# Kernel optimization log

Hardware: AMD Instinct MI355X
Metric: run time of the kernel (lower is better)

The kernel has to match this reference:

```python
import jax, jax.numpy as jnp
import numpy as np

N_ENT = 100000
N_REL = 100
DIM = 128
N_BASES = 10
N_LAYERS = 2
N_EDGES = 600000


def setup_inputs() -> dict:
    key = jax.random.key(0)
    ks = jax.random.split(key, 8)
    source = jax.random.randint(ks[0], (N_EDGES,), 0, N_ENT)
    target = jax.random.randint(ks[1], (N_EDGES,), 0, N_ENT)
    edge_type = jax.random.randint(ks[2], (N_EDGES,), 0, N_REL)
    x0 = jax.random.normal(ks[3], (N_ENT, DIM), dtype=jnp.float32)
    bases = jax.random.normal(ks[4], (N_BASES, DIM, DIM), dtype=jnp.float32) * (DIM ** -0.5)
    coefs = jax.random.normal(ks[5], (N_LAYERS, N_REL, N_BASES), dtype=jnp.float32) * (N_BASES ** -0.5)
    self_w = jax.random.normal(ks[6], (N_LAYERS, DIM, DIM), dtype=jnp.float32) * (DIM ** -0.5)
    bias = jnp.zeros((N_LAYERS, DIM), dtype=jnp.float32)
    return {"x0": x0, "bases": bases, "coefs": coefs, "self_w": self_w,
            "bias": bias, "source": source, "target": target, "edge_type": edge_type}


def reference(x0, bases, coefs, self_w, bias, source, target, edge_type):
    """R-GCN entity representations (basis decomposition, inverse in-degree norm).

    x0: (N, d) base entity embeddings; bases: (B, d, d); coefs: (L, R, B);
    self_w: (L, d, d); bias: (L, d); source/target/edge_type: (E,) int.
    Returns (N, d) entity representations after L layers.
    """
    n = x0.shape[0]
    n_layers = coefs.shape[0]
    n_bases = bases.shape[0]
    # inverse in-degree edge weights: w_e = 1 / indegree(target_e)
    indeg = jax.ops.segment_sum(jnp.ones_like(target, dtype=x0.dtype), target, num_segments=n)
    ew = (1.0 / jnp.maximum(indeg, 1.0))[target]  # (E,)
    x = x0
    for l in range(n_layers):
        xs = x[source]                         # (E, d) gather
        ecoef = coefs[l][edge_type]            # (E, B) relation-specific basis coefficients
        msg = jnp.zeros_like(xs)
        for b in range(n_bases):               # small fixed loop over bases
            msg = msg + ecoef[:, b:b + 1] * (xs @ bases[b])
        agg = jax.ops.segment_sum(ew[:, None] * msg, target, num_segments=n)  # (N, d)
        x = jax.nn.relu(agg + x @ self_w[l] + bias[l])
    return x
```

## Files before the change

### kernel.cpp

```cpp
#include <hip/hip_runtime.h>

#define NENT    100000
#define NENTPAD 100096
#define NREL    100
#define DIM     128
#define NBASES  10
#define NEDGES  600000
#define CH      128
#define TMAX    4788
#define PADE    612736
#define NB_ESCAN 98
#define EPB     4096
#define NBH     147
#define NPERS   512

typedef unsigned short u16;
typedef unsigned int   u32;
typedef __bf16  bf16x8 __attribute__((ext_vector_type(8)));
typedef float   f32x16 __attribute__((ext_vector_type(16)));

static __device__ __forceinline__ u16 f2bf(float f) {
  u32 u = __float_as_uint(f);
  u = (u + 0x7fffu + ((u >> 16) & 1u)) >> 16;
  return (u16)u;
}
static __device__ __forceinline__ float bf2f(u32 h) {
  return __uint_as_float(h << 16);
}
static __device__ __forceinline__ u32 pk2(float a, float b) {
  return (u32)f2bf(a) | ((u32)f2bf(b) << 16);
}
#define GLD16(g, l) __builtin_amdgcn_global_load_lds( \
    (__attribute__((address_space(1))) u32*)(g), \
    (__attribute__((address_space(3))) u32*)(l), 16, 0, 0)

__global__ __launch_bounds__(1024) void k_hist2(const int* __restrict__ tgt,
                                                const int* __restrict__ rel,
                                                int* __restrict__ indeg,
                                                int* __restrict__ hist) {
  __shared__ int h[NREL];
  int tid = threadIdx.x, blk = blockIdx.x;
  if (tid < NREL) h[tid] = 0;
  __syncthreads();
  int base = blk * EPB;
  int nv = NEDGES - base; if (nv > EPB) nv = EPB;
#pragma unroll
  for (int k = 0; k < 4; ++k) {
    int j = tid + k * 1024;
    if (j < nv) {
      int i = base + j;
      atomicAdd(&indeg[tgt[i]], 1);
      atomicAdd(&h[rel[i]], 1);
    }
  }
  __syncthreads();
  if (tid < NREL) hist[tid * NBH + blk] = h[tid];
}

__global__ __launch_bounds__(1024) void k_scan2(int* __restrict__ hist,
                                                int* __restrict__ chunk_rel,
                                                int* __restrict__ chunk_start,
                                                int* __restrict__ chunk_valid,
                                                int* __restrict__ chunkT) {
  __shared__ int sh[NREL * NBH];
  __shared__ int cnt[NREL];
  __shared__ int cb[128];
  int tid = threadIdx.x;
  for (int i = tid; i < NREL * NBH; i += 1024) sh[i] = hist[i];
  __syncthreads();
  if (tid < NREL) {
    int s = 0;
    for (int b = 0; b < NBH; ++b) s += sh[tid * NBH + b];
    cnt[tid] = s;
  }
  __syncthreads();
  if (tid < 128) cb[tid] = (tid < NREL) ? (cnt[tid] + CH - 1) / CH : 0;
  __syncthreads();
  for (int d = 1; d < 128; d <<= 1) {
    int t = 0;
    if (tid < 128 && tid >= d) t = cb[tid - d];
    __syncthreads();
    if (tid < 128) cb[tid] += t;
    __syncthreads();
  }
  if (tid < NREL) {
    int c = cnt[tid];
    int nch = (c + CH - 1) / CH;
    int cb0 = cb[tid] - nch;
    int poff = cb0 * CH;
    for (int i = 0; i < nch; ++i) {
      chunk_rel[cb0 + i] = tid;
      chunk_start[cb0 + i] = (cb0 + i) * CH;
      int v = c - i * CH;
      if (v > CH) v = CH;
      chunk_valid[cb0 + i] = v;
    }
    int run = poff;
    for (int b = 0; b < NBH; ++b) {
      int t = sh[tid * NBH + b];
      sh[tid * NBH + b] = run;
      run += t;
    }
  }
  if (tid == 127) *chunkT = cb[127];
  __syncthreads();
  for (int i = tid; i < NREL * NBH; i += 1024) hist[i] = sh[i];
}

__global__ __launch_bounds__(1024) void k_scatter2(const int* __restrict__ src,
                                                   const int* __restrict__ tgt,
                                                   const int* __restrict__ rel,
                                                   const int* __restrict__ hist,
                                                   const int* __restrict__ row_ptr,
                                                   int* __restrict__ fill_t,
                                                   int* __restrict__ es,
                                                   int* __restrict__ tp) {
  __shared__ int lh[NREL];
  __shared__ int lc[NREL];
  __shared__ int goff[NREL];
  __shared__ int ls[128];
  __shared__ int es_l[EPB];
  __shared__ int tp_l[EPB];
  __shared__ int dst_l[EPB];
  int tid = threadIdx.x, blk = blockIdx.x;
  int base = blk * EPB;
  int nv = NEDGES - base; if (nv > EPB) nv = EPB;
  if (tid < NREL) {
    lh[tid] = 0; lc[tid] = 0;
    goff[tid] = hist[tid * NBH + blk];
  }
  __syncthreads();
  int r4[4], s4[4], t4[4];
#pragma unroll
  for (int k = 0; k < 4; ++k) {
    int j = tid + k * 1024;
    if (j < nv) {
      int i = base + j;
      r4[k] = rel[i]; s4[k] = src[i]; t4[k] = tgt[i];
      atomicAdd(&lh[r4[k]], 1);
    } else r4[k] = -1;
  }
  __syncthreads();
  if (tid < 128) ls[tid] = (tid < NREL) ? lh[tid] : 0;
  __syncthreads();
  for (int d = 1; d < 128; d <<= 1) {
    int t = 0;
    if (tid < 128 && tid >= d) t = ls[tid - d];
    __syncthreads();
    if (tid < 128) ls[tid] += t;
    __syncthreads();
  }
#pragma unroll
  for (int k = 0; k < 4; ++k) {
    if (r4[k] >= 0) {
      int r = r4[k];
      int rank = atomicAdd(&lc[r], 1);
      int lpos = ls[r] - lh[r] + rank;
      es_l[lpos] = s4[k];
      dst_l[lpos] = goff[r] + rank;
      tp_l[lpos] = row_ptr[t4[k]] + atomicAdd(&fill_t[t4[k]], 1);
    }
  }
  __syncthreads();
  for (int j = tid; j < nv; j += 1024) {
    int d = dst_l[j];
    es[d] = es_l[j];
    tp[d] = tp_l[j];
  }
}

__global__ void k_escanA(const int* __restrict__ indeg, int* __restrict__ loc,
                         int* __restrict__ bsum) {
  __shared__ int s[256];
  int tid = threadIdx.x;
  int base = blockIdx.x * 1024 + tid * 4;
  int v0 = (base + 0 < NENT) ? indeg[base + 0] : 0;
  int v1 = (base + 1 < NENT) ? indeg[base + 1] : 0;
  int v2 = (base + 2 < NENT) ? indeg[base + 2] : 0;
  int v3 = (base + 3 < NENT) ? indeg[base + 3] : 0;
  s[tid] = v0 + v1 + v2 + v3;
  __syncthreads();
  for (int d = 1; d < 256; d <<= 1) {
    int t = (tid >= d) ? s[tid - d] : 0;
    __syncthreads();
    s[tid] += t;
    __syncthreads();
  }
  int off = (tid > 0) ? s[tid - 1] : 0;
  if (base + 0 < NENT) loc[base + 0] = off;
  if (base + 1 < NENT) loc[base + 1] = off + v0;
  if (base + 2 < NENT) loc[base + 2] = off + v0 + v1;
  if (base + 3 < NENT) loc[base + 3] = off + v0 + v1 + v2;
  if (tid == 255) bsum[blockIdx.x] = s[255];
}

__global__ void k_escanB(int* __restrict__ bsum) {
  __shared__ int s[128];
  int tid = threadIdx.x;
  s[tid] = (tid < NB_ESCAN) ? bsum[tid] : 0;
  __syncthreads();
  for (int d = 1; d < 128; d <<= 1) {
    int t = (tid >= d) ? s[tid - d] : 0;
    __syncthreads();
    s[tid] += t;
    __syncthreads();
  }
  if (tid < NB_ESCAN) bsum[tid] = (tid > 0) ? s[tid - 1] : 0;
}

__global__ void k_escanC(const int* __restrict__ loc, const int* __restrict__ bsum,
                         int* __restrict__ row_ptr) {
  int i = blockIdx.x * blockDim.x + threadIdx.x;
  if (i < NENT) row_ptr[i] = loc[i] + bsum[i >> 10];
}

__global__ void k_tobf(const float* __restrict__ x, u16* __restrict__ xbf) {
  int t = blockIdx.x * 256 + threadIdx.x;
  int row = t >> 4, g = t & 15;
  int c = g ^ (row & 7);
  const float4* xr = (const float4*)(x + (size_t)row * DIM + c * 8);
  float4 a = xr[0], b = xr[1];
  uint4 o;
  o.x = pk2(a.x, a.y); o.y = pk2(a.z, a.w);
  o.z = pk2(b.x, b.y); o.w = pk2(b.z, b.w);
  *(uint4*)(xbf + (size_t)row * DIM + g * 8) = o;
}

__global__ void k_wmatT(const float* __restrict__ bases, const float* __restrict__ coefs_l,
                        u16* __restrict__ Wt) {
  int g = blockIdx.x * 256 + threadIdx.x;
  int r = g >> 11;
  int rem = g & 2047;
  int k8 = rem >> 7;
  int dim = rem & 127;
  float cf[NBASES];
#pragma unroll
  for (int bb = 0; bb < NBASES; ++bb) cf[bb] = coefs_l[r * NBASES + bb];
  float v[8];
#pragma unroll
  for (int i = 0; i < 8; ++i) v[i] = 0.f;
  for (int bb = 0; bb < NBASES; ++bb) {
    const float* bp = bases + (size_t)bb * DIM * DIM + (k8 * 8) * DIM + dim;
#pragma unroll
    for (int i = 0; i < 8; ++i) v[i] += cf[bb] * bp[i * DIM];
  }
  uint4 o;
  o.x = pk2(v[0], v[1]); o.y = pk2(v[2], v[3]);
  o.z = pk2(v[4], v[5]); o.w = pk2(v[6], v[7]);
  *(uint4*)(Wt + (size_t)r * DIM * DIM + dim * DIM + ((k8 ^ (dim & 7)) * 8)) = o;
}

__global__ void k_swtT(const float* __restrict__ sw, u16* __restrict__ swt) {
  int g = blockIdx.x * 256 + threadIdx.x;
  int ll = g >> 11;
  int rem = g & 2047;
  int k8 = rem >> 7;
  int dim = rem & 127;
  const float* bp = sw + (size_t)ll * DIM * DIM + (k8 * 8) * DIM + dim;
  float v[8];
#pragma unroll
  for (int i = 0; i < 8; ++i) v[i] = bp[i * DIM];
  uint4 o;
  o.x = pk2(v[0], v[1]); o.y = pk2(v[2], v[3]);
  o.z = pk2(v[4], v[5]); o.w = pk2(v[6], v[7]);
  *(uint4*)(swt + (size_t)ll * DIM * DIM + dim * DIM + ((k8 ^ (dim & 7)) * 8)) = o;
}

__launch_bounds__(512, 2)
__global__ void k_edgeP(const u16* __restrict__ xbf, const u16* __restrict__ Wt,
                        const int* __restrict__ es, const int* __restrict__ tp,
                        const int* __restrict__ chunk_rel, const int* __restrict__ chunk_start,
                        const int* __restrict__ chunk_valid, const int* __restrict__ chunkT,
                        u16* __restrict__ msg) {
  __shared__ __align__(16) char smem[65536];
  int nch = *chunkT;
  int K = (nch + NPERS - 1) / NPERS;
  int c0 = blockIdx.x * K;
  int c1 = c0 + K; if (c1 > nch) c1 = nch;
  if (c0 >= nch) return;
  int tid = threadIdx.x;
  int w = tid >> 6, l = tid & 63;
  int lr = l & 31, hi = l >> 5;
  int dt = w & 3;
  int d = dt * 32 + lr;
  int e1 = (w >> 2) * 32 + lr;
  int aswz = d & 7, bswz = lr & 7;
  const char* wb = smem;
  const char* xb = smem + 32768;
  int curR = -1;
  for (int cb = c0; cb < c1; ++cb) {
    int r = chunk_rel[cb], base = chunk_start[cb], nv = chunk_valid[cb];
    __syncthreads();
    if (r != curR) {
      const char* wg = (const char*)(Wt + (size_t)r * DIM * DIM);
#pragma unroll
      for (int it = 0; it < 4; ++it) {
        int off = it * 8192 + tid * 16;
        GLD16(wg + off, smem + off);
      }
      curR = r;
    }
    {
      int e = tid >> 2, q = tid & 3;
      int sidx = (e < nv) ? es[base + e] : 0;
      const char* xr = (const char*)(xbf + (size_t)sidx * DIM);
      char* xd = smem + 32768 + e * 256;
      int xk = (sidx & 7) ^ (e & 7);
#pragma unroll
      for (int i = 0; i < 4; ++i) {
        int g = q * 4 + i;
        uint4 v = *(const uint4*)(xr + g * 16);
        *(uint4*)(xd + ((g ^ xk) * 16)) = v;
      }
    }
    __syncthreads();
    f32x16 accA, accB;
#pragma unroll
    for (int i = 0; i < 16; ++i) { accA[i] = 0.f; accB[i] = 0.f; }
#pragma unroll
    for (int s = 0; s < 8; ++s) {
      int c = s * 2 + hi;
      bf16x8 av = *(const bf16x8*)(wb + d * 256 + ((c ^ aswz) * 16));
      bf16x8 b1 = *(const bf16x8*)(xb + e1 * 256 + ((c ^ bswz) * 16));
      bf16x8 b2 = *(const bf16x8*)(xb + (e1 + 64) * 256 + ((c ^ bswz) * 16));
      accA = __builtin_amdgcn_mfma_f32_32x32x16_bf16(av, b1, accA, 0, 0, 0);
      accB = __builtin_amdgcn_mfma_f32_32x32x16_bf16(av, b2, accB, 0, 0, 0);
    }
#pragma unroll
    for (int t = 0; t < 2; ++t) {
      int e = e1 + t * 64;
      if (e < nv) {
        int p = tp[base + e];
        u16* mrow = msg + (size_t)p * DIM + dt * 32 + hi * 16;
#pragma unroll
        for (int half = 0; half < 2; ++half) {
          float v0 = t ? accB[8 * half + 0] : accA[8 * half + 0];
          float v1 = t ? accB[8 * half + 1] : accA[8 * half + 1];
          float v2 = t ? accB[8 * half + 2] : accA[8 * half + 2];
          float v3 = t ? accB[8 * half + 3] : accA[8 * half + 3];
          float v4 = t ? accB[8 * half + 4] : accA[8 * half + 4];
          float v5 = t ? accB[8 * half + 5] : accA[8 * half + 5];
          float v6 = t ? accB[8 * half + 6] : accA[8 * half + 6];
          float v7 = t ? accB[8 * half + 7] : accA[8 * half + 7];
          uint4 o;
          o.x = pk2(v0, v1); o.y = pk2(v2, v3);
          o.z = pk2(v4, v5); o.w = pk2(v6, v7);
          *(uint4*)(mrow + 8 * half) = o;
        }
      }
    }
  }
}

#define ACC8(M, B_) \
  ms[(B_) + 0] += bf2f((M).x & 0xffffu); ms[(B_) + 1] += bf2f((M).x >> 16); \
  ms[(B_) + 2] += bf2f((M).y & 0xffffu); ms[(B_) + 3] += bf2f((M).y >> 16); \
  ms[(B_) + 4] += bf2f((M).z & 0xffffu); ms[(B_) + 5] += bf2f((M).z >> 16); \
  ms[(B_) + 6] += bf2f((M).w & 0xffffu); ms[(B_) + 7] += bf2f((M).w >> 16);

__launch_bounds__(512, 4)
__global__ void k_combM(const u16* __restrict__ xbf, const u16* __restrict__ swt,
                        const float* __restrict__ bias_l, const u16* __restrict__ msg,
                        const int* __restrict__ row_ptr, const int* __restrict__ indeg,
                        float* __restrict__ outf, u16* __restrict__ outb, int last) {
  __shared__ __align__(16) char smem[65536];
  int tid = threadIdx.x;
  int r0 = blockIdx.x * 128;
  {
    const char* wg = (const char*)swt;
    const char* xg = (const char*)(xbf + (size_t)r0 * DIM);
#pragma unroll
    for (int it = 0; it < 4; ++it) {
      int off = it * 8192 + tid * 16;
      GLD16(wg + off, smem + off);
      GLD16(xg + off, smem + 32768 + off);
    }
  }
  __syncthreads();
  int w = tid >> 6, l = tid & 63;
  int lr = l & 31, hi = l >> 5;
  int dt = w & 3;
  int d = dt * 32 + lr;
  int e1 = (w >> 2) * 32 + lr;
  const char* wb = smem;
  const char* xb = smem + 32768;
  f32x16 accA, accB;
#pragma unroll
  for (int i = 0; i < 16; ++i) { accA[i] = 0.f; accB[i] = 0.f; }
  int aswz = d & 7, bswz = lr & 7;
#pragma unroll
  for (int s = 0; s < 8; ++s) {
    int c = s * 2 + hi;
    bf16x8 av = *(const bf16x8*)(wb + d * 256 + ((c ^ aswz) * 16));
    bf16x8 b1 = *(const bf16x8*)(xb + e1 * 256 + ((c ^ bswz) * 16));
    bf16x8 b2 = *(const bf16x8*)(xb + (e1 + 64) * 256 + ((c ^ bswz) * 16));
    accA = __builtin_amdgcn_mfma_f32_32x32x16_bf16(av, b1, accA, 0, 0, 0);
    accB = __builtin_amdgcn_mfma_f32_32x32x16_bf16(av, b2, accB, 0, 0, 0);
  }
#pragma unroll
  for (int t = 0; t < 2; ++t) {
    int ent = r0 + e1 + t * 64;
    int vald = (ent < NENT);
    int eb = vald ? row_ptr[ent] : 0;
    int dg = vald ? indeg[ent] : 0;
    float inv = 1.f / (float)(dg > 1 ? dg : 1);
    float ms[16];
#pragma unroll
    for (int i = 0; i < 16; ++i) ms[i] = 0.f;
    const u16* mp = msg + (size_t)eb * DIM + dt * 32 + hi * 16;
    int j = 0;
    for (; j + 1 < dg; j += 2) {
      uint4 m1 = *(const uint4*)(mp);
      uint4 m2 = *(const uint4*)(mp + 8);
      uint4 m3 = *(const uint4*)(mp + DIM);
      uint4 m4 = *(const uint4*)(mp + DIM + 8);
      ACC8(m1, 0) ACC8(m2, 8) ACC8(m3, 0) ACC8(m4, 8)
      mp += 2 * DIM;
    }
    if (j < dg) {
      uint4 m1 = *(const uint4*)(mp);
      uint4 m2 = *(const uint4*)(mp + 8);
      ACC8(m1, 0) ACC8(m2, 8)
    }
    if (vald) {
#pragma unroll
      for (int q = 0; q < 4; ++q) {
        float4 bi = *(const float4*)(bias_l + dt * 32 + hi * 4 + 8 * q);
        float a0 = t ? accB[4 * q + 0] : accA[4 * q + 0];
        float a1 = t ? accB[4 * q + 1] : accA[4 * q + 1];
        float a2 = t ? accB[4 * q + 2] : accA[4 * q + 2];
        float a3 = t ? accB[4 * q + 3] : accA[4 * q + 3];
        float o0 = fmaxf(ms[4 * q + 0] * inv + a0 + bi.x, 0.f);
        float o1 = fmaxf(ms[4 * q + 1] * inv + a1 + bi.y, 0.f);
        float o2 = fmaxf(ms[4 * q + 2] * inv + a2 + bi.z, 0.f);
        float o3 = fmaxf(ms[4 * q + 3] * inv + a3 + bi.w, 0.f);
        if (last) {
          float4 o = make_float4(o0, o1, o2, o3);
          *(float4*)(outf + (size_t)ent * DIM + dt * 32 + hi * 4 + 8 * q) = o;
        } else {
          int c16 = 4 * dt + q;
          uint2 o;
          o.x = pk2(o0, o1); o.y = pk2(o2, o3);
          *(uint2*)(outb + (size_t)ent * DIM + ((c16 ^ (ent & 7)) * 8) + 4 * hi) = o;
        }
      }
    }
  }
}

extern "C" void kernel_launch(void* const* d_in, const int* in_sizes, int n_in,
                              void* d_out, int out_size, void* d_ws, size_t ws_size,
                              hipStream_t stream) {
  const float* x0    = (const float*)d_in[0];
  const float* bases = (const float*)d_in[1];
  const float* coefs = (const float*)d_in[2];
  const float* selfw = (const float*)d_in[3];
  const float* bias  = (const float*)d_in[4];
  const int* src = (const int*)d_in[5];
  const int* tgt = (const int*)d_in[6];
  const int* rel = (const int*)d_in[7];
  float* out = (float*)d_out;

  char* ws = (char*)d_ws;
  size_t off = 0;
  auto alloc = [&](size_t bytes) -> void* {
    void* p = ws + off;
    off = (off + bytes + 255) & ~(size_t)255;
    return p;
  };
  u16* Wt   = (u16*)alloc((size_t)NREL * DIM * DIM * 2);
  u16* swt  = (u16*)alloc((size_t)2 * DIM * DIM * 2);
  u16* xbf  = (u16*)alloc((size_t)NENTPAD * DIM * 2);
  u16* msg  = (u16*)alloc((size_t)NEDGES * DIM * 2);
  int* es      = (int*)alloc((size_t)PADE * sizeof(int));
  int* tp      = (int*)alloc((size_t)PADE * sizeof(int));
  int* indeg   = (int*)alloc((size_t)NENT * sizeof(int));
  int* row_ptr = (int*)alloc((size_t)NENT * sizeof(int));
  int* loc     = (int*)alloc((size_t)NENT * sizeof(int));
  int* fill_t  = (int*)alloc((size_t)NENT * sizeof(int));
  int* bsum    = (int*)alloc(128 * sizeof(int));
  int* hist    = (int*)alloc((size_t)NREL * NBH * sizeof(int));
  int* chunk_rel   = (int*)alloc(TMAX * sizeof(int));
  int* chunk_start = (int*)alloc(TMAX * sizeof(int));
  int* chunk_valid = (int*)alloc(TMAX * sizeof(int));
  int* chunkT      = (int*)alloc(sizeof(int));

  hipMemsetAsync(indeg, 0, (size_t)NENT * sizeof(int), stream);
  hipMemsetAsync(fill_t, 0, (size_t)NENT * sizeof(int), stream);

  k_hist2<<<NBH, 1024, 0, stream>>>(tgt, rel, indeg, hist);
  k_scan2<<<1, 1024, 0, stream>>>(hist, chunk_rel, chunk_start, chunk_valid, chunkT);
  k_escanA<<<NB_ESCAN, 256, 0, stream>>>(indeg, loc, bsum);
  k_escanB<<<1, 128, 0, stream>>>(bsum);
  k_escanC<<<(NENT + 255) / 256, 256, 0, stream>>>(loc, bsum, row_ptr);
  k_scatter2<<<NBH, 1024, 0, stream>>>(src, tgt, rel, hist, row_ptr, fill_t, es, tp);
  k_tobf<<<(NENT * 16) / 256, 256, 0, stream>>>(x0, xbf);
  k_swtT<<<16, 256, 0, stream>>>(selfw, swt);

  for (int l = 0; l < 2; ++l) {
    k_wmatT<<<(NREL * 2048) / 256, 256, 0, stream>>>(bases, coefs + l * NREL * NBASES, Wt);
    k_edgeP<<<NPERS, 512, 0, stream>>>(xbf, Wt, es, tp,
                                       chunk_rel, chunk_start, chunk_valid, chunkT, msg);
    k_combM<<<NENTPAD / 128, 512, 0, stream>>>(xbf, swt + (size_t)l * DIM * DIM,
                                               bias + l * DIM, msg, row_ptr, indeg,
                                               out, xbf, l == 0 ? 0 : 1);
  }
}
```

Before: 322.5 us.

## Halve edge chunk size, use 256-thread edge blocks, fold block-sum scan into escanC

The edge-message kernel now works on 64-edge chunks with 256 threads (4 waves, each wave owning 32 output dims across 64 edges). It runs more persistent blocks with less shared memory, and target indices are prefetched before the barrier. This cuts padding waste from partially filled per-relation chunks and raises occupancy. The cost is more chunks and more reloads of the relation weight matrix. Separately, the single-block scan of block sums is merged into k_escanC, where every block redoes the small scan, removing one kernel launch.

```diff
diff --git a/kernel.cpp b/kernel.cpp
--- a/kernel.cpp
+++ b/kernel.cpp
@@ -6,13 +6,13 @@
 #define DIM     128
 #define NBASES  10
 #define NEDGES  600000
-#define CH      128
-#define TMAX    4788
-#define PADE    612736
+#define CH      64
+#define TMAX    9600
+#define PADE    606336
 #define NB_ESCAN 98
 #define EPB     4096
 #define NBH     147
-#define NPERS   512
+#define NPERS   768
 
 typedef unsigned short u16;
 typedef unsigned int   u32;
@@ -194,24 +194,24 @@
   if (tid == 255) bsum[blockIdx.x] = s[255];
 }
 
-__global__ void k_escanB(int* __restrict__ bsum) {
-  __shared__ int s[128];
-  int tid = threadIdx.x;
-  s[tid] = (tid < NB_ESCAN) ? bsum[tid] : 0;
-  __syncthreads();
-  for (int d = 1; d < 128; d <<= 1) {
-    int t = (tid >= d) ? s[tid - d] : 0;
-    __syncthreads();
-    s[tid] += t;
-    __syncthreads();
-  }
-  if (tid < NB_ESCAN) bsum[tid] = (tid > 0) ? s[tid - 1] : 0;
-}
-
 __global__ void k_escanC(const int* __restrict__ loc, const int* __restrict__ bsum,
                          int* __restrict__ row_ptr) {
-  int i = blockIdx.x * blockDim.x + threadIdx.x;
-  if (i < NENT) row_ptr[i] = loc[i] + bsum[i >> 10];
+  __shared__ int sb[128];
+  int tid = threadIdx.x;
+  if (tid < 128) sb[tid] = (tid < NB_ESCAN) ? bsum[tid] : 0;
+  __syncthreads();
+  for (int d = 1; d < 128; d <<= 1) {
+    int t = 0;
+    if (tid < 128 && tid >= d) t = sb[tid - d];
+    __syncthreads();
+    if (tid < 128) sb[tid] += t;
+    __syncthreads();
+  }
+  int i = blockIdx.x * 256 + tid;
+  if (i < NENT) {
+    int b = i >> 10;
+    row_ptr[i] = loc[i] + (b > 0 ? sb[b - 1] : 0);
+  }
 }
 
 __global__ void k_tobf(const float* __restrict__ x, u16* __restrict__ xbf) {
@@ -266,13 +266,13 @@
   *(uint4*)(swt + (size_t)ll * DIM * DIM + dim * DIM + ((k8 ^ (dim & 7)) * 8)) = o;
 }
 
-__launch_bounds__(512, 2)
+__launch_bounds__(256, 3)
 __global__ void k_edgeP(const u16* __restrict__ xbf, const u16* __restrict__ Wt,
                         const int* __restrict__ es, const int* __restrict__ tp,
                         const int* __restrict__ chunk_rel, const int* __restrict__ chunk_start,
                         const int* __restrict__ chunk_valid, const int* __restrict__ chunkT,
                         u16* __restrict__ msg) {
-  __shared__ __align__(16) char smem[65536];
+  __shared__ __align__(16) char smem[49152];
   int nch = *chunkT;
   int K = (nch + NPERS - 1) / NPERS;
   int c0 = blockIdx.x * K;
@@ -281,9 +281,7 @@
   int tid = threadIdx.x;
   int w = tid >> 6, l = tid & 63;
   int lr = l & 31, hi = l >> 5;
-  int dt = w & 3;
-  int d = dt * 32 + lr;
-  int e1 = (w >> 2) * 32 + lr;
+  int d = w * 32 + lr;
   int aswz = d & 7, bswz = lr & 7;
   const char* wb = smem;
   const char* xb = smem + 32768;
@@ -294,8 +292,8 @@
     if (r != curR) {
       const char* wg = (const char*)(Wt + (size_t)r * DIM * DIM);
 #pragma unroll
-      for (int it = 0; it < 4; ++it) {
-        int off = it * 8192 + tid * 16;
+      for (int it = 0; it < 8; ++it) {
+        int off = it * 4096 + tid * 16;
         GLD16(wg + off, smem + off);
       }
       curR = r;
@@ -313,6 +311,8 @@
         *(uint4*)(xd + ((g ^ xk) * 16)) = v;
       }
     }
+    int pA = (lr < nv) ? tp[base + lr] : 0;
+    int pB = (lr + 32 < nv) ? tp[base + lr + 32] : 0;
     __syncthreads();
     f32x16 accA, accB;
 #pragma unroll
@@ -321,17 +321,17 @@
     for (int s = 0; s < 8; ++s) {
       int c = s * 2 + hi;
       bf16x8 av = *(const bf16x8*)(wb + d * 256 + ((c ^ aswz) * 16));
-      bf16x8 b1 = *(const bf16x8*)(xb + e1 * 256 + ((c ^ bswz) * 16));
-      bf16x8 b2 = *(const bf16x8*)(xb + (e1 + 64) * 256 + ((c ^ bswz) * 16));
+      bf16x8 b1 = *(const bf16x8*)(xb + lr * 256 + ((c ^ bswz) * 16));
+      bf16x8 b2 = *(const bf16x8*)(xb + (lr + 32) * 256 + ((c ^ bswz) * 16));
       accA = __builtin_amdgcn_mfma_f32_32x32x16_bf16(av, b1, accA, 0, 0, 0);
       accB = __builtin_amdgcn_mfma_f32_32x32x16_bf16(av, b2, accB, 0, 0, 0);
     }
 #pragma unroll
     for (int t = 0; t < 2; ++t) {
-      int e = e1 + t * 64;
+      int e = lr + t * 32;
       if (e < nv) {
-        int p = tp[base + e];
-        u16* mrow = msg + (size_t)p * DIM + dt * 32 + hi * 16;
+        int p = t ? pB : pA;
+        u16* mrow = msg + (size_t)p * DIM + w * 32 + hi * 16;
 #pragma unroll
         for (int half = 0; half < 2; ++half) {
           float v0 = t ? accB[8 * half + 0] : accA[8 * half + 0];
@@ -491,7 +491,6 @@
   k_hist2<<<NBH, 1024, 0, stream>>>(tgt, rel, indeg, hist);
   k_scan2<<<1, 1024, 0, stream>>>(hist, chunk_rel, chunk_start, chunk_valid, chunkT);
   k_escanA<<<NB_ESCAN, 256, 0, stream>>>(indeg, loc, bsum);
-  k_escanB<<<1, 128, 0, stream>>>(bsum);
   k_escanC<<<(NENT + 255) / 256, 256, 0, stream>>>(loc, bsum, row_ptr);
   k_scatter2<<<NBH, 1024, 0, stream>>>(src, tgt, rel, hist, row_ptr, fill_t, es, tp);
   k_tobf<<<(NENT * 16) / 256, 256, 0, stream>>>(x0, xbf);
@@ -499,7 +498,7 @@
 
   for (int l = 0; l < 2; ++l) {
     k_wmatT<<<(NREL * 2048) / 256, 256, 0, stream>>>(bases, coefs + l * NREL * NBASES, Wt);
-    k_edgeP<<<NPERS, 512, 0, stream>>>(xbf, Wt, es, tp,
+    k_edgeP<<<NPERS, 256, 0, stream>>>(xbf, Wt, es, tp,
                                        chunk_rel, chunk_start, chunk_valid, chunkT, msg);
     k_combM<<<NENTPAD / 128, 512, 0, stream>>>(xbf, swt + (size_t)l * DIM * DIM,
                                                bias + l * DIM, msg, row_ptr, indeg,
```

Result: no change. 328.4 us (+1.8%).

## Prefetch next chunk's gathered rows in registers during MFMA; fold block-sum scan into escanC

Applied to the files above, without the earlier changes.

The edge-message kernel now gathers the next chunk's source rows into registers while the current chunk runs its MFMA loop. It stores them to shared memory after a barrier, hiding global gather latency behind compute, and also loads the target positions before the MFMA loop. Separately, the single-block scan of block sums is merged into k_escanC, with each block redoing the small scan, which removes one kernel launch. The cost is higher register pressure from four uint4 prefetch registers and redundant scan work in every escanC block.

```diff
diff --git a/kernel.cpp b/kernel.cpp
--- a/kernel.cpp
+++ b/kernel.cpp
@@ -194,24 +194,24 @@
   if (tid == 255) bsum[blockIdx.x] = s[255];
 }
 
-__global__ void k_escanB(int* __restrict__ bsum) {
-  __shared__ int s[128];
-  int tid = threadIdx.x;
-  s[tid] = (tid < NB_ESCAN) ? bsum[tid] : 0;
-  __syncthreads();
-  for (int d = 1; d < 128; d <<= 1) {
-    int t = (tid >= d) ? s[tid - d] : 0;
-    __syncthreads();
-    s[tid] += t;
-    __syncthreads();
-  }
-  if (tid < NB_ESCAN) bsum[tid] = (tid > 0) ? s[tid - 1] : 0;
-}
-
 __global__ void k_escanC(const int* __restrict__ loc, const int* __restrict__ bsum,
                          int* __restrict__ row_ptr) {
-  int i = blockIdx.x * blockDim.x + threadIdx.x;
-  if (i < NENT) row_ptr[i] = loc[i] + bsum[i >> 10];
+  __shared__ int sb[128];
+  int tid = threadIdx.x;
+  if (tid < 128) sb[tid] = (tid < NB_ESCAN) ? bsum[tid] : 0;
+  __syncthreads();
+  for (int d = 1; d < 128; d <<= 1) {
+    int t = 0;
+    if (tid < 128 && tid >= d) t = sb[tid - d];
+    __syncthreads();
+    if (tid < 128) sb[tid] += t;
+    __syncthreads();
+  }
+  int i = blockIdx.x * 256 + tid;
+  if (i < NENT) {
+    int b = i >> 10;
+    row_ptr[i] = loc[i] + (b > 0 ? sb[b - 1] : 0);
+  }
 }
 
 __global__ void k_tobf(const float* __restrict__ x, u16* __restrict__ xbf) {
@@ -287,33 +287,51 @@
   int aswz = d & 7, bswz = lr & 7;
   const char* wb = smem;
   const char* xb = smem + 32768;
+  int eS = tid >> 2, q = tid & 3;
+  char* xd = smem + 32768 + eS * 256;
   int curR = -1;
+  int nbase = chunk_start[c0], nnv = chunk_valid[c0], nrel = chunk_rel[c0];
+  uint4 vr0, vr1, vr2, vr3;
+  int xk;
+  {
+    int sidx = (eS < nnv) ? es[nbase + eS] : 0;
+    const char* xr = (const char*)(xbf + (size_t)sidx * DIM);
+    vr0 = *(const uint4*)(xr + (q * 4 + 0) * 16);
+    vr1 = *(const uint4*)(xr + (q * 4 + 1) * 16);
+    vr2 = *(const uint4*)(xr + (q * 4 + 2) * 16);
+    vr3 = *(const uint4*)(xr + (q * 4 + 3) * 16);
+    xk = (sidx & 7) ^ (eS & 7);
+  }
+  {
+    const char* wg = (const char*)(Wt + (size_t)nrel * DIM * DIM);
+#pragma unroll
+    for (int it = 0; it < 4; ++it) {
+      int off = it * 8192 + tid * 16;
+      GLD16(wg + off, smem + off);
+    }
+    curR = nrel;
+  }
+  *(uint4*)(xd + (((q * 4 + 0) ^ xk) * 16)) = vr0;
+  *(uint4*)(xd + (((q * 4 + 1) ^ xk) * 16)) = vr1;
+  *(uint4*)(xd + (((q * 4 + 2) ^ xk) * 16)) = vr2;
+  *(uint4*)(xd + (((q * 4 + 3) ^ xk) * 16)) = vr3;
+  __syncthreads();
+
   for (int cb = c0; cb < c1; ++cb) {
-    int r = chunk_rel[cb], base = chunk_start[cb], nv = chunk_valid[cb];
-    __syncthreads();
-    if (r != curR) {
-      const char* wg = (const char*)(Wt + (size_t)r * DIM * DIM);
-#pragma unroll
-      for (int it = 0; it < 4; ++it) {
-        int off = it * 8192 + tid * 16;
-        GLD16(wg + off, smem + off);
-      }
-      curR = r;
-    }
-    {
-      int e = tid >> 2, q = tid & 3;
-      int sidx = (e < nv) ? es[base + e] : 0;
+    int base = nbase, nv = nnv;
+    int havenext = (cb + 1 < c1);
+    if (havenext) {
+      nbase = chunk_start[cb + 1]; nnv = chunk_valid[cb + 1]; nrel = chunk_rel[cb + 1];
+      int sidx = (eS < nnv) ? es[nbase + eS] : 0;
       const char* xr = (const char*)(xbf + (size_t)sidx * DIM);
-      char* xd = smem + 32768 + e * 256;
-      int xk = (sidx & 7) ^ (e & 7);
-#pragma unroll
-      for (int i = 0; i < 4; ++i) {
-        int g = q * 4 + i;
-        uint4 v = *(const uint4*)(xr + g * 16);
-        *(uint4*)(xd + ((g ^ xk) * 16)) = v;
-      }
-    }
-    __syncthreads();
+      vr0 = *(const uint4*)(xr + (q * 4 + 0) * 16);
+      vr1 = *(const uint4*)(xr + (q * 4 + 1) * 16);
+      vr2 = *(const uint4*)(xr + (q * 4 + 2) * 16);
+      vr3 = *(const uint4*)(xr + (q * 4 + 3) * 16);
+      xk = (sidx & 7) ^ (eS & 7);
+    }
+    int pA = (e1 < nv) ? tp[base + e1] : 0;
+    int pB = (e1 + 64 < nv) ? tp[base + e1 + 64] : 0;
     f32x16 accA, accB;
 #pragma unroll
     for (int i = 0; i < 16; ++i) { accA[i] = 0.f; accB[i] = 0.f; }
@@ -330,7 +348,7 @@
     for (int t = 0; t < 2; ++t) {
       int e = e1 + t * 64;
       if (e < nv) {
-        int p = tp[base + e];
+        int p = t ? pB : pA;
         u16* mrow = msg + (size_t)p * DIM + dt * 32 + hi * 16;
 #pragma unroll
         for (int half = 0; half < 2; ++half) {
@@ -349,6 +367,23 @@
         }
       }
     }
+    __syncthreads();
+    if (havenext) {
+      if (nrel != curR) {
+        const char* wg = (const char*)(Wt + (size_t)nrel * DIM * DIM);
+#pragma unroll
+        for (int it = 0; it < 4; ++it) {
+          int off = it * 8192 + tid * 16;
+          GLD16(wg + off, smem + off);
+        }
+        curR = nrel;
+      }
+      *(uint4*)(xd + (((q * 4 + 0) ^ xk) * 16)) = vr0;
+      *(uint4*)(xd + (((q * 4 + 1) ^ xk) * 16)) = vr1;
+      *(uint4*)(xd + (((q * 4 + 2) ^ xk) * 16)) = vr2;
+      *(uint4*)(xd + (((q * 4 + 3) ^ xk) * 16)) = vr3;
+    }
+    __syncthreads();
   }
 }
 
@@ -491,7 +526,6 @@
   k_hist2<<<NBH, 1024, 0, stream>>>(tgt, rel, indeg, hist);
   k_scan2<<<1, 1024, 0, stream>>>(hist, chunk_rel, chunk_start, chunk_valid, chunkT);
   k_escanA<<<NB_ESCAN, 256, 0, stream>>>(indeg, loc, bsum);
-  k_escanB<<<1, 128, 0, stream>>>(bsum);
   k_escanC<<<(NENT + 255) / 256, 256, 0, stream>>>(loc, bsum, row_ptr);
   k_scatter2<<<NBH, 1024, 0, stream>>>(src, tgt, rel, hist, row_ptr, fill_t, es, tp);
   k_tobf<<<(NENT * 16) / 256, 256, 0, stream>>>(x0, xbf);
```

Measured after the change: 322.2 us. About the same (-0.1%).
